# Performance work log

Hardware: AMD Instinct MI355X
Metric: run time of the kernel (lower is better)

Reference implementation:

```python
import jax, jax.numpy as jnp
import numpy as np

B, S, D, H = 8, 1024, 1024, 16
DH = D // H  # 64
SCALE = (DH // H) ** (-0.5)  # faithful to torch: (key.size(-1) // num_heads) ** -0.5 = 4**-0.5 = 0.5
LN_EPS = 1e-5


def setup_inputs() -> dict:
    key = jax.random.key(0)
    ks = jax.random.split(key, 12)
    f = jnp.float32
    return {
        "key":   jax.random.normal(ks[0], (B, S, D), f),
        "value": jax.random.normal(ks[1], (B, S, D), f),
        "query": jax.random.normal(ks[2], (B, S, D), f),
        "Wq": jax.random.normal(ks[3], (D, D), f) * 0.02,
        "bq": jnp.zeros((D,), f),
        "Wk": jax.random.normal(ks[4], (D, D), f) * 0.02,
        "bk": jnp.zeros((D,), f),
        "Wv": jax.random.normal(ks[5], (D, D), f) * 0.02,
        "bv": jnp.zeros((D,), f),
        "Wo": jax.random.normal(ks[6], (D, D), f) * 0.02,
        "bo": jnp.zeros((D,), f),
        "ln_gamma": jnp.ones((D,), f),
        "ln_beta": jnp.zeros((D,), f),
    }


def _layer_norm(x, gamma, beta):
    mu = jnp.mean(x, axis=-1, keepdims=True)
    var = jnp.mean(jnp.square(x - mu), axis=-1, keepdims=True)
    return (x - mu) * jax.lax.rsqrt(var + LN_EPS) * gamma + beta


def reference(key, value, query, Wq, bq, Wk, bk, Wv, bv, Wo, bo, ln_gamma, ln_beta):
    residual = query
    # QKV projections (torch Linear: x @ W.T + b)
    k = key @ Wk.T + bk
    v = value @ Wv.T + bv
    q = query @ Wq.T + bq
    # Faithful raw view [B,S,H*dh] -> [B*H, S, dh] (row-major reshape, as in torch .view)
    k = k.reshape(B * H, S, DH)
    v = v.reshape(B * H, S, DH)
    q = q.reshape(B * H, S, DH)
    # scores: [B*H, S, S], softmax over last axis (dim=2)
    attn = jnp.einsum("bid,bjd->bij", q, k) * SCALE
    attn = jax.nn.softmax(attn, axis=2)
    context = jnp.einsum("bij,bjd->bid", attn, v)
    context = context.reshape(B, S, D)  # faithful raw view back
    out = context @ Wo.T + bo
    out = _layer_norm(residual + out, ln_gamma, ln_beta)
    return out, attn
```

## Files before the change

### kernel.cpp

```cpp
#include <hip/hip_runtime.h>
#include <stdint.h>

typedef unsigned short ushort_t;
typedef __attribute__((ext_vector_type(8))) short s16x8;
typedef __attribute__((ext_vector_type(8))) unsigned short u16x8;
typedef __attribute__((ext_vector_type(4))) unsigned short u16x4;
typedef __attribute__((ext_vector_type(4))) float f32x4;

#define AS1C(p) ((const __attribute__((address_space(1))) void*)(p))
#define AS3(p)  ((__attribute__((address_space(3))) void*)(p))

#define QSCALE 0.7213475204444817f

#define EXP2F(x) __builtin_amdgcn_exp2f(x)
#define LOG2F(x) __builtin_amdgcn_logf(x)

#define WAVE_LDS_FENCE()                                    \
  do {                                                      \
    asm volatile("s_waitcnt lgkmcnt(0)" ::: "memory");      \
    __builtin_amdgcn_sched_barrier(0);                      \
  } while (0)

#define SBAR()                                              \
  do {                                                      \
    __builtin_amdgcn_sched_barrier(0);                      \
    __builtin_amdgcn_s_barrier();                           \
    __builtin_amdgcn_sched_barrier(0);                      \
  } while (0)

__device__ __forceinline__ ushort_t f2bf(float f) {
  uint32_t u = __float_as_uint(f);
  u += 0x7fffu + ((u >> 16) & 1u);
  return (ushort_t)(u >> 16);
}
__device__ __forceinline__ float bf2f(ushort_t h) {
  return __uint_as_float(((uint32_t)h) << 16);
}

__global__ __launch_bounds__(256) void cvt3_kernel(const float* __restrict__ s0,
                                                   const float* __restrict__ s1,
                                                   const float* __restrict__ s2,
                                                   ushort_t* __restrict__ dst) {
  const int y = blockIdx.y;
  const float* src = y == 0 ? s0 : (y == 1 ? s1 : s2);
  const int i = blockIdx.x * 256 + threadIdx.x;
  const float4 v = ((const float4*)src)[i];
  ushort4 o;
  o.x = f2bf(v.x); o.y = f2bf(v.y); o.z = f2bf(v.z); o.w = f2bf(v.w);
  ((ushort4*)(dst + (size_t)y * 8388608))[i] = o;
}

__global__ __launch_bounds__(256) void cvtw_kernel(const float* __restrict__ w0,
                                                   const float* __restrict__ w1,
                                                   const float* __restrict__ w2,
                                                   const float* __restrict__ w3,
                                                   ushort_t* __restrict__ dqkv,
                                                   ushort_t* __restrict__ dwo) {
  const int y = blockIdx.y;
  const float* src = y == 0 ? w0 : (y == 1 ? w1 : (y == 2 ? w2 : w3));
  ushort_t* dst = y < 3 ? dqkv + (size_t)y * 1048576 : dwo;
  const float sc = y == 0 ? QSCALE : 1.0f;
  const int i = blockIdx.x * 256 + threadIdx.x;
  const float4 v = ((const float4*)src)[i];
  ushort4 o;
  o.x = f2bf(v.x * sc); o.y = f2bf(v.y * sc); o.z = f2bf(v.z * sc); o.w = f2bf(v.w * sc);
  ((ushort4*)dst)[i] = o;
}

__global__ __launch_bounds__(256) void biascat_kernel(const float* __restrict__ bq,
                                                      const float* __restrict__ bk,
                                                      const float* __restrict__ bv,
                                                      float* __restrict__ dst) {
  const int i = blockIdx.x * 256 + threadIdx.x;
  dst[i] = i < 1024 ? bq[i] * QSCALE : (i < 2048 ? bk[i - 1024] : bv[i - 2048]);
}

template <int OUT_BF16>
__global__ __launch_bounds__(256) void gemm_nt(const ushort_t* __restrict__ A0,
                                               const ushort_t* __restrict__ A1,
                                               const ushort_t* __restrict__ A2,
                                               const ushort_t* __restrict__ B,
                                               const float* __restrict__ bias,
                                               void* __restrict__ C0,
                                               void* __restrict__ C1,
                                               void* __restrict__ C2) {
  __shared__ ushort_t As[2][128 * 32];
  __shared__ ushort_t Bs[2][128 * 32];
  const int tid = threadIdx.x;
  const int w = tid >> 6, lane = tid & 63, g = lane >> 4, c = lane & 15;
  const int wm = w >> 1, wn = w & 1;
  const int m0 = blockIdx.y * 128, n0 = blockIdx.x * 128;
  const int sel = n0 >> 10, nloc0 = n0 & 1023;
  const ushort_t* A = sel == 0 ? A0 : (sel == 1 ? A1 : A2);
  char* C = (char*)(sel == 0 ? C0 : (sel == 1 ? C1 : C2));
  f32x4 acc[4][4] = {};

  const int row0 = tid >> 2, col0 = (tid & 3) << 3;
  const int row1 = (256 + tid) >> 2, col1 = ((256 + tid) & 3) << 3;
  const int dst0 = (0 * 256 + w * 64) * 8, dst1 = (1 * 256 + w * 64) * 8;

#define G_STAGE(buf, k0_)                                                                  \
  do {                                                                                     \
    __builtin_amdgcn_global_load_lds(AS1C(&A[(size_t)(m0 + row0) * 1024 + (k0_) + col0]),  \
                                     AS3(&As[buf][dst0]), 16, 0, 0);                       \
    __builtin_amdgcn_global_load_lds(AS1C(&B[(size_t)(n0 + row0) * 1024 + (k0_) + col0]),  \
                                     AS3(&Bs[buf][dst0]), 16, 0, 0);                       \
    __builtin_amdgcn_global_load_lds(AS1C(&A[(size_t)(m0 + row1) * 1024 + (k0_) + col1]),  \
                                     AS3(&As[buf][dst1]), 16, 0, 0);                       \
    __builtin_amdgcn_global_load_lds(AS1C(&B[(size_t)(n0 + row1) * 1024 + (k0_) + col1]),  \
                                     AS3(&Bs[buf][dst1]), 16, 0, 0);                       \
  } while (0)

  G_STAGE(0, 0);
  asm volatile("s_waitcnt vmcnt(0)" ::: "memory");
  SBAR();
  for (int it = 0; it < 32; ++it) {
    const int cur = it & 1;
    if (it < 31) G_STAGE(cur ^ 1, 32 * (it + 1));
    s16x8 af[4], bfr[4];
#pragma unroll
    for (int mi = 0; mi < 4; ++mi)
      af[mi] = *(const s16x8*)&As[cur][(wm * 64 + mi * 16 + c) * 32 + g * 8];
#pragma unroll
    for (int ni = 0; ni < 4; ++ni)
      bfr[ni] = *(const s16x8*)&Bs[cur][(wn * 64 + ni * 16 + c) * 32 + g * 8];
    __builtin_amdgcn_s_setprio(1);
#pragma unroll
    for (int mi = 0; mi < 4; ++mi)
#pragma unroll
      for (int ni = 0; ni < 4; ++ni)
        acc[mi][ni] = __builtin_amdgcn_mfma_f32_16x16x32_bf16(af[mi], bfr[ni], acc[mi][ni], 0, 0, 0);
    __builtin_amdgcn_s_setprio(0);
    asm volatile("s_waitcnt vmcnt(0) lgkmcnt(0)" ::: "memory");
    SBAR();
  }
#undef G_STAGE

#pragma unroll
  for (int ni = 0; ni < 4; ++ni) {
    const int nn = wn * 64 + ni * 16 + c;
    const float bv = bias[n0 + nn];
#pragma unroll
    for (int mi = 0; mi < 4; ++mi) {
#pragma unroll
      for (int rr = 0; rr < 4; ++rr) {
        const int m = m0 + wm * 64 + mi * 16 + g * 4 + rr;
        const float val = acc[mi][ni][rr] + bv;
        if (OUT_BF16)
          ((ushort_t*)C)[(size_t)m * 1024 + nloc0 + nn] = f2bf(val);
        else
          ((float*)C)[(size_t)m * 1024 + nloc0 + nn] = val;
      }
    }
  }
}

__global__ __launch_bounds__(256) void transpose_v(const ushort_t* __restrict__ v,
                                                   ushort_t* __restrict__ vt) {
  __shared__ ushort_t T[64][72];
  const int n = blockIdx.y, ib = blockIdx.x;
  const int t = threadIdx.x;
  {
    const int row = t >> 2, cb = (t & 3) << 4;
    const ushort_t* src = v + (size_t)n * 65536 + (size_t)(ib * 64 + row) * 64 + cb;
    *(u16x8*)&T[row][cb] = *(const u16x8*)src;
    *(u16x8*)&T[row][cb + 8] = *(const u16x8*)(src + 8);
  }
  __syncthreads();
  {
    const int dh = t >> 2, ibs = (t & 3) << 4;
    u16x8 a, b;
#pragma unroll
    for (int e = 0; e < 8; ++e) { a[e] = T[ibs + e][dh]; b[e] = T[ibs + 8 + e][dh]; }
    ushort_t* dst = vt + (size_t)n * 65536 + (size_t)dh * 1024 + ib * 64 + ibs;
    *(u16x8*)dst = a;
    *(u16x8*)(dst + 8) = b;
  }
}

__global__ __launch_bounds__(256) void attn_kernel(const ushort_t* __restrict__ q,
                                                   const ushort_t* __restrict__ k,
                                                   const ushort_t* __restrict__ vt,
                                                   float* __restrict__ attn,
                                                   ushort_t* __restrict__ ctx) {
  __shared__ ushort_t Kb[2][64 * 64];
  __shared__ ushort_t Vb[2][64 * 64];
  __shared__ ushort_t Pb[4][16 * 64];
  const int wg = blockIdx.x;
  const int idx = ((wg & 7) << 8) | (wg >> 3);
  const int n = idx >> 4, qb = idx & 15;
  const int tid = threadIdx.x, w = tid >> 6, lane = tid & 63, g = lane >> 4, c = lane & 15;
  const int i0 = qb * 64 + w * 16;
  const ushort_t* qh = q + (size_t)n * 65536;
  const char* khb = (const char*)(k + (size_t)n * 65536);
  const char* vhb = (const char*)(vt + (size_t)n * 65536);
  char* pwb = (char*)&Pb[w][0];

  const int r0 = w * 16 + (lane >> 3);
  const int csw = (((lane & 7) ^ (lane >> 3)) << 4);

#define STAGE_K(buf, jt_)                                                                   \
  do {                                                                                      \
    __builtin_amdgcn_global_load_lds(AS1C(khb + ((size_t)(jt_)*64 + r0) * 128 + csw),       \
                                     AS3(&Kb[buf][(w * 2 + 0) * 512]), 16, 0, 0);           \
    __builtin_amdgcn_global_load_lds(AS1C(khb + ((size_t)(jt_)*64 + r0 + 8) * 128 + csw),   \
                                     AS3(&Kb[buf][(w * 2 + 1) * 512]), 16, 0, 0);           \
  } while (0)
#define STAGE_V(buf, jt_)                                                                   \
  do {                                                                                      \
    __builtin_amdgcn_global_load_lds(AS1C(vhb + (size_t)r0 * 2048 + (jt_)*128 + csw),       \
                                     AS3(&Vb[buf][(w * 2 + 0) * 512]), 16, 0, 0);           \
    __builtin_amdgcn_global_load_lds(AS1C(vhb + (size_t)(r0 + 8) * 2048 + (jt_)*128 + csw), \
                                     AS3(&Vb[buf][(w * 2 + 1) * 512]), 16, 0, 0);           \
  } while (0)
#define KFRAG(buf, jn, h)                                                     \
  (*(const s16x8*)((const char*)&Kb[buf][0] +                                 \
                   (((((jn)*16 + c) * 128 + (h)*64 + g * 16)) ^ ((c & 7) << 4))))
#define VFRAG(buf, dn, ks_)                                                   \
  (*(const s16x8*)((const char*)&Vb[buf][0] +                                 \
                   (((((dn)*16 + c) * 128 + (ks_)*64 + g * 16)) ^ ((c & 7) << 4))))

  const s16x8 aq0 = *(const s16x8*)&qh[(i0 + c) * 64 + g * 8];
  const s16x8 aq1 = *(const s16x8*)&qh[(i0 + c) * 64 + 32 + g * 8];

  float m_p[4], l_p[4];
#pragma unroll
  for (int r = 0; r < 4; ++r) { m_p[r] = -1e30f; l_p[r] = 0.f; }

  STAGE_K(0, 0);
  asm volatile("s_waitcnt vmcnt(0)" ::: "memory");
  SBAR();
  for (int jt = 0; jt < 16; ++jt) {
    const int cur = jt & 1;
    if (jt < 15) STAGE_K(cur ^ 1, jt + 1);
    f32x4 s[4];
    __builtin_amdgcn_s_setprio(1);
#pragma unroll
    for (int jn = 0; jn < 4; ++jn) {
      f32x4 z = {0.f, 0.f, 0.f, 0.f};
      z = __builtin_amdgcn_mfma_f32_16x16x32_bf16(aq0, KFRAG(cur, jn, 0), z, 0, 0, 0);
      z = __builtin_amdgcn_mfma_f32_16x16x32_bf16(aq1, KFRAG(cur, jn, 1), z, 0, 0, 0);
      s[jn] = z;
    }
    __builtin_amdgcn_s_setprio(0);
#pragma unroll
    for (int r = 0; r < 4; ++r) {
      const float pm = fmaxf(fmaxf(s[0][r], s[1][r]), fmaxf(s[2][r], s[3][r]));
      const float mn = fmaxf(m_p[r], pm);
      l_p[r] = l_p[r] * EXP2F(m_p[r] - mn) + EXP2F(s[0][r] - mn) + EXP2F(s[1][r] - mn) +
               EXP2F(s[2][r] - mn) + EXP2F(s[3][r] - mn);
      m_p[r] = mn;
    }
    if (jt < 15) {
      asm volatile("s_waitcnt vmcnt(0) lgkmcnt(0)" ::: "memory");
      SBAR();
    }
  }

  float bias_r[4];
#pragma unroll
  for (int r = 0; r < 4; ++r) {
    float m = m_p[r], l = l_p[r];
#pragma unroll
    for (int mask = 1; mask < 16; mask <<= 1) {
      const float mo = __shfl_xor(m, mask);
      const float lo = __shfl_xor(l, mask);
      const float mn = fmaxf(m, mo);
      l = l * EXP2F(m - mn) + lo * EXP2F(mo - mn);
      m = mn;
    }
    bias_r[r] = m + LOG2F(l);
  }

  f32x4 cacc[4] = {};
  float* arow = attn + (size_t)n * 1048576;

  STAGE_K(0, 0);
  STAGE_V(0, 0);
  asm volatile("s_waitcnt vmcnt(0) lgkmcnt(0)" ::: "memory");
  SBAR();
  for (int jt = 0; jt < 16; ++jt) {
    const int cur = jt & 1;
    if (jt < 15) { STAGE_K(cur ^ 1, jt + 1); STAGE_V(cur ^ 1, jt + 1); }
    f32x4 s[4];
    __builtin_amdgcn_s_setprio(1);
#pragma unroll
    for (int jn = 0; jn < 4; ++jn) {
      f32x4 z = {0.f, 0.f, 0.f, 0.f};
      z = __builtin_amdgcn_mfma_f32_16x16x32_bf16(aq0, KFRAG(cur, jn, 0), z, 0, 0, 0);
      z = __builtin_amdgcn_mfma_f32_16x16x32_bf16(aq1, KFRAG(cur, jn, 1), z, 0, 0, 0);
      s[jn] = z;
    }
    __builtin_amdgcn_s_setprio(0);
#pragma unroll
    for (int jn = 0; jn < 4; ++jn) {
#pragma unroll
      for (int r = 0; r < 4; ++r) {
        const float p = EXP2F(s[jn][r] - bias_r[r]);
        const int row = 4 * g + r;
        const int A = (row << 7) + ((jn * 16 + c) << 1);
        *(ushort_t*)(pwb + (A ^ ((row & 7) << 4))) = f2bf(p);
      }
    }
    WAVE_LDS_FENCE();
    __builtin_amdgcn_s_setprio(1);
#pragma unroll
    for (int ks = 0; ks < 2; ++ks) {
      const int A = (c << 7) + (ks << 6) + (g << 4);
      const s16x8 pa = *(const s16x8*)(pwb + (A ^ ((c & 7) << 4)));
#pragma unroll
      for (int dn = 0; dn < 4; ++dn)
        cacc[dn] = __builtin_amdgcn_mfma_f32_16x16x32_bf16(pa, VFRAG(cur, dn, ks), cacc[dn], 0, 0, 0);
    }
    __builtin_amdgcn_s_setprio(0);
#pragma unroll
    for (int e = 0; e < 4; ++e) {
      const int row = g + 4 * e;
      const int A = (row << 7) + (c << 3);
      const u16x4 hv = *(const u16x4*)(pwb + (A ^ ((row & 7) << 4)));
      f32x4 fv;
#pragma unroll
      for (int t2 = 0; t2 < 4; ++t2) fv[t2] = bf2f(hv[t2]);
      *(f32x4*)&arow[(size_t)(i0 + row) * 1024 + jt * 64 + c * 4] = fv;
    }
    if (jt < 15) {
      asm volatile("s_waitcnt vmcnt(4) lgkmcnt(0)" ::: "memory");
      SBAR();
    }
  }

  ushort_t* ch = ctx + (size_t)n * 65536;
#pragma unroll
  for (int dn = 0; dn < 4; ++dn)
#pragma unroll
    for (int r = 0; r < 4; ++r)
      ch[(size_t)(i0 + 4 * g + r) * 64 + dn * 16 + c] = f2bf(cacc[dn][r]);
#undef STAGE_K
#undef STAGE_V
#undef KFRAG
#undef VFRAG
}

__global__ __launch_bounds__(256) void ln_kernel(const float* __restrict__ proj,
                                                 const float* __restrict__ resid,
                                                 const float* __restrict__ gamma,
                                                 const float* __restrict__ beta,
                                                 float* __restrict__ out) {
  __shared__ float sred[4], ssred[4];
  const int row = blockIdx.x, t = threadIdx.x;
  const float4 pv = ((const float4*)(proj + (size_t)row * 1024))[t];
  const float4 rv = ((const float4*)(resid + (size_t)row * 1024))[t];
  float4 x;
  x.x = pv.x + rv.x; x.y = pv.y + rv.y; x.z = pv.z + rv.z; x.w = pv.w + rv.w;
  float s = x.x + x.y + x.z + x.w;
  float ss = x.x * x.x + x.y * x.y + x.z * x.z + x.w * x.w;
#pragma unroll
  for (int msk = 1; msk < 64; msk <<= 1) {
    s += __shfl_xor(s, msk);
    ss += __shfl_xor(ss, msk);
  }
  const int w = t >> 6, lane = t & 63;
  if (lane == 0) { sred[w] = s; ssred[w] = ss; }
  __syncthreads();
  s = sred[0] + sred[1] + sred[2] + sred[3];
  ss = ssred[0] + ssred[1] + ssred[2] + ssred[3];
  const float mu = s * (1.f / 1024.f);
  const float var = ss * (1.f / 1024.f) - mu * mu;
  const float rs = rsqrtf(var + 1e-5f);
  const float4 gm = ((const float4*)gamma)[t];
  const float4 bt = ((const float4*)beta)[t];
  float4 o;
  o.x = (x.x - mu) * rs * gm.x + bt.x;
  o.y = (x.y - mu) * rs * gm.y + bt.y;
  o.z = (x.z - mu) * rs * gm.z + bt.z;
  o.w = (x.w - mu) * rs * gm.w + bt.w;
  ((float4*)(out + (size_t)row * 1024))[t] = o;
}

extern "C" void kernel_launch(void* const* d_in, const int* in_sizes, int n_in,
                              void* d_out, int out_size, void* d_ws, size_t ws_size,
                              hipStream_t stream) {
  const float* key   = (const float*)d_in[0];
  const float* value = (const float*)d_in[1];
  const float* query = (const float*)d_in[2];
  const float* Wq = (const float*)d_in[3];  const float* bq = (const float*)d_in[4];
  const float* Wk = (const float*)d_in[5];  const float* bk = (const float*)d_in[6];
  const float* Wv = (const float*)d_in[7];  const float* bv = (const float*)d_in[8];
  const float* Wo = (const float*)d_in[9];  const float* bo = (const float*)d_in[10];
  const float* gamma = (const float*)d_in[11];
  const float* beta  = (const float*)d_in[12];

  char* ws = (char*)d_ws;
  ushort_t* q_   = (ushort_t*)(ws + 0);
  ushort_t* k_   = (ushort_t*)(ws + 16777216);
  ushort_t* vt_  = (ushort_t*)(ws + 33554432);
  ushort_t* ctx_ = (ushort_t*)(ws + 50331648);
  ushort_t* wo_  = (ushort_t*)(ws + 67108864);
  float*    proj_ = (float*)(ws + 0);

  char* o8 = (char*)d_out;
  float*    outp  = (float*)o8;
  float*    attnp = (float*)(o8 + 33554432);
  ushort_t* xq   = (ushort_t*)(o8 + 33554432);
  ushort_t* xk   = (ushort_t*)(o8 + 50331648);
  ushort_t* xv   = (ushort_t*)(o8 + 67108864);
  ushort_t* wqkv = (ushort_t*)(o8 + 83886080);
  ushort_t* v_   = (ushort_t*)(o8 + 90177536);
  float*    bqkv = (float*)(o8 + 106954752);

  cvt3_kernel<<<dim3(8192, 3), 256, 0, stream>>>(query, key, value, xq);
  cvtw_kernel<<<dim3(1024, 4), 256, 0, stream>>>(Wq, Wk, Wv, Wo, wqkv, wo_);
  biascat_kernel<<<12, 256, 0, stream>>>(bq, bk, bv, bqkv);

  gemm_nt<1><<<dim3(24, 64), 256, 0, stream>>>(xq, xk, xv, wqkv, bqkv, q_, k_, v_);

  transpose_v<<<dim3(16, 128), 256, 0, stream>>>(v_, vt_);

  attn_kernel<<<2048, 256, 0, stream>>>(q_, k_, vt_, attnp, ctx_);

  gemm_nt<0><<<dim3(8, 64), 256, 0, stream>>>(ctx_, ctx_, ctx_, wo_, bo, proj_, proj_, proj_);

  ln_kernel<<<8192, 256, 0, stream>>>(proj_, query, gamma, beta, outp);
}
```

Measured before the change: 361.3 us.

## Split attention keys across waves with single-pass softmax; triple-buffer GEMM loads

The attention kernel now gives each workgroup 16 query rows and splits the 1024 keys across four waves, 256 keys per wave. Each wave keeps all of its scores in registers, so the score GEMM runs once instead of twice for the two-pass softmax. Row max and sum are combined across waves through LDS, and partial context sums are reduced through LDS before the bf16 store. K and V are now read straight from global memory rather than staged in LDS, and the grid grows to 8192 blocks. Separately, the GEMM moves from double to triple buffering so loads run two stages ahead, at the cost of more LDS and register pressure.

```diff
diff --git a/kernel.cpp b/kernel.cpp
--- a/kernel.cpp
+++ b/kernel.cpp
@@ -84,8 +84,8 @@
                                                void* __restrict__ C0,
                                                void* __restrict__ C1,
                                                void* __restrict__ C2) {
-  __shared__ ushort_t As[2][128 * 32];
-  __shared__ ushort_t Bs[2][128 * 32];
+  __shared__ ushort_t As[3][128 * 32];
+  __shared__ ushort_t Bs[3][128 * 32];
   const int tid = threadIdx.x;
   const int w = tid >> 6, lane = tid & 63, g = lane >> 4, c = lane & 15;
   const int wm = w >> 1, wn = w & 1;
@@ -112,11 +112,15 @@
   } while (0)
 
   G_STAGE(0, 0);
-  asm volatile("s_waitcnt vmcnt(0)" ::: "memory");
+  G_STAGE(1, 32);
+  asm volatile("s_waitcnt vmcnt(4)" ::: "memory");
   SBAR();
+  int cur = 0;
   for (int it = 0; it < 32; ++it) {
-    const int cur = it & 1;
-    if (it < 31) G_STAGE(cur ^ 1, 32 * (it + 1));
+    if (it < 30) {
+      const int sb = cur >= 1 ? cur - 1 : 2;
+      G_STAGE(sb, 32 * (it + 2));
+    }
     s16x8 af[4], bfr[4];
 #pragma unroll
     for (int mi = 0; mi < 4; ++mi)
@@ -131,8 +135,14 @@
       for (int ni = 0; ni < 4; ++ni)
         acc[mi][ni] = __builtin_amdgcn_mfma_f32_16x16x32_bf16(af[mi], bfr[ni], acc[mi][ni], 0, 0, 0);
     __builtin_amdgcn_s_setprio(0);
-    asm volatile("s_waitcnt vmcnt(0) lgkmcnt(0)" ::: "memory");
-    SBAR();
+    if (it < 31) {
+      if (it < 30)
+        asm volatile("s_waitcnt vmcnt(4) lgkmcnt(0)" ::: "memory");
+      else
+        asm volatile("s_waitcnt vmcnt(0) lgkmcnt(0)" ::: "memory");
+      SBAR();
+    }
+    cur = cur < 2 ? cur + 1 : 0;
   }
 #undef G_STAGE
 
@@ -183,162 +193,137 @@
                                                    const ushort_t* __restrict__ vt,
                                                    float* __restrict__ attn,
                                                    ushort_t* __restrict__ ctx) {
-  __shared__ ushort_t Kb[2][64 * 64];
-  __shared__ ushort_t Vb[2][64 * 64];
-  __shared__ ushort_t Pb[4][16 * 64];
+  __shared__ char Lds[4][8192];
+  __shared__ float mlb[4][16][2];
   const int wg = blockIdx.x;
-  const int idx = ((wg & 7) << 8) | (wg >> 3);
-  const int n = idx >> 4, qb = idx & 15;
+  const int idx = ((wg & 7) << 10) | (wg >> 3);
+  const int n = idx >> 6, qb = idx & 63;
   const int tid = threadIdx.x, w = tid >> 6, lane = tid & 63, g = lane >> 4, c = lane & 15;
-  const int i0 = qb * 64 + w * 16;
+  const int i0 = qb * 16;
+  const int cb = w << 8;
   const ushort_t* qh = q + (size_t)n * 65536;
-  const char* khb = (const char*)(k + (size_t)n * 65536);
-  const char* vhb = (const char*)(vt + (size_t)n * 65536);
-  char* pwb = (char*)&Pb[w][0];
-
-  const int r0 = w * 16 + (lane >> 3);
-  const int csw = (((lane & 7) ^ (lane >> 3)) << 4);
-
-#define STAGE_K(buf, jt_)                                                                   \
-  do {                                                                                      \
-    __builtin_amdgcn_global_load_lds(AS1C(khb + ((size_t)(jt_)*64 + r0) * 128 + csw),       \
-                                     AS3(&Kb[buf][(w * 2 + 0) * 512]), 16, 0, 0);           \
-    __builtin_amdgcn_global_load_lds(AS1C(khb + ((size_t)(jt_)*64 + r0 + 8) * 128 + csw),   \
-                                     AS3(&Kb[buf][(w * 2 + 1) * 512]), 16, 0, 0);           \
-  } while (0)
-#define STAGE_V(buf, jt_)                                                                   \
-  do {                                                                                      \
-    __builtin_amdgcn_global_load_lds(AS1C(vhb + (size_t)r0 * 2048 + (jt_)*128 + csw),       \
-                                     AS3(&Vb[buf][(w * 2 + 0) * 512]), 16, 0, 0);           \
-    __builtin_amdgcn_global_load_lds(AS1C(vhb + (size_t)(r0 + 8) * 2048 + (jt_)*128 + csw), \
-                                     AS3(&Vb[buf][(w * 2 + 1) * 512]), 16, 0, 0);           \
-  } while (0)
-#define KFRAG(buf, jn, h)                                                     \
-  (*(const s16x8*)((const char*)&Kb[buf][0] +                                 \
-                   (((((jn)*16 + c) * 128 + (h)*64 + g * 16)) ^ ((c & 7) << 4))))
-#define VFRAG(buf, dn, ks_)                                                   \
-  (*(const s16x8*)((const char*)&Vb[buf][0] +                                 \
-                   (((((dn)*16 + c) * 128 + (ks_)*64 + g * 16)) ^ ((c & 7) << 4))))
+  const ushort_t* kh = k + (size_t)n * 65536;
+  const ushort_t* vh = vt + (size_t)n * 65536;
+  char* pwb = &Lds[w][0];
 
   const s16x8 aq0 = *(const s16x8*)&qh[(i0 + c) * 64 + g * 8];
   const s16x8 aq1 = *(const s16x8*)&qh[(i0 + c) * 64 + 32 + g * 8];
 
-  float m_p[4], l_p[4];
-#pragma unroll
-  for (int r = 0; r < 4; ++r) { m_p[r] = -1e30f; l_p[r] = 0.f; }
-
-  STAGE_K(0, 0);
-  asm volatile("s_waitcnt vmcnt(0)" ::: "memory");
-  SBAR();
-  for (int jt = 0; jt < 16; ++jt) {
-    const int cur = jt & 1;
-    if (jt < 15) STAGE_K(cur ^ 1, jt + 1);
-    f32x4 s[4];
-    __builtin_amdgcn_s_setprio(1);
-#pragma unroll
-    for (int jn = 0; jn < 4; ++jn) {
-      f32x4 z = {0.f, 0.f, 0.f, 0.f};
-      z = __builtin_amdgcn_mfma_f32_16x16x32_bf16(aq0, KFRAG(cur, jn, 0), z, 0, 0, 0);
-      z = __builtin_amdgcn_mfma_f32_16x16x32_bf16(aq1, KFRAG(cur, jn, 1), z, 0, 0, 0);
-      s[jn] = z;
-    }
-    __builtin_amdgcn_s_setprio(0);
+  f32x4 s[16];
+#pragma unroll
+  for (int jn = 0; jn < 16; ++jn) {
+    const ushort_t* kr = &kh[(size_t)(cb + jn * 16 + c) * 64];
+    f32x4 z = {0.f, 0.f, 0.f, 0.f};
+    z = __builtin_amdgcn_mfma_f32_16x16x32_bf16(aq0, *(const s16x8*)&kr[g * 8], z, 0, 0, 0);
+    z = __builtin_amdgcn_mfma_f32_16x16x32_bf16(aq1, *(const s16x8*)&kr[32 + g * 8], z, 0, 0, 0);
+    s[jn] = z;
+  }
+
+  float bias_r[4];
+  {
+    float mr[4], lr[4];
 #pragma unroll
     for (int r = 0; r < 4; ++r) {
-      const float pm = fmaxf(fmaxf(s[0][r], s[1][r]), fmaxf(s[2][r], s[3][r]));
-      const float mn = fmaxf(m_p[r], pm);
-      l_p[r] = l_p[r] * EXP2F(m_p[r] - mn) + EXP2F(s[0][r] - mn) + EXP2F(s[1][r] - mn) +
-               EXP2F(s[2][r] - mn) + EXP2F(s[3][r] - mn);
-      m_p[r] = mn;
-    }
-    if (jt < 15) {
-      asm volatile("s_waitcnt vmcnt(0) lgkmcnt(0)" ::: "memory");
-      SBAR();
-    }
-  }
-
-  float bias_r[4];
-#pragma unroll
-  for (int r = 0; r < 4; ++r) {
-    float m = m_p[r], l = l_p[r];
-#pragma unroll
-    for (int mask = 1; mask < 16; mask <<= 1) {
-      const float mo = __shfl_xor(m, mask);
-      const float lo = __shfl_xor(l, mask);
-      const float mn = fmaxf(m, mo);
-      l = l * EXP2F(m - mn) + lo * EXP2F(mo - mn);
-      m = mn;
-    }
-    bias_r[r] = m + LOG2F(l);
-  }
+      float m = s[0][r];
+#pragma unroll
+      for (int jn = 1; jn < 16; ++jn) m = fmaxf(m, s[jn][r]);
+      m = fmaxf(m, __shfl_xor(m, 1));
+      m = fmaxf(m, __shfl_xor(m, 2));
+      m = fmaxf(m, __shfl_xor(m, 4));
+      m = fmaxf(m, __shfl_xor(m, 8));
+      float l = 0.f;
+#pragma unroll
+      for (int jn = 0; jn < 16; ++jn) l += EXP2F(s[jn][r] - m);
+      l += __shfl_xor(l, 1);
+      l += __shfl_xor(l, 2);
+      l += __shfl_xor(l, 4);
+      l += __shfl_xor(l, 8);
+      mr[r] = m; lr[r] = l;
+    }
+    if (c == 0) {
+#pragma unroll
+      for (int r = 0; r < 4; ++r) {
+        mlb[w][4 * g + r][0] = mr[r];
+        mlb[w][4 * g + r][1] = lr[r];
+      }
+    }
+    WAVE_LDS_FENCE();
+    SBAR();
+#pragma unroll
+    for (int r = 0; r < 4; ++r) {
+      const int row = 4 * g + r;
+      float M = fmaxf(fmaxf(mlb[0][row][0], mlb[1][row][0]),
+                      fmaxf(mlb[2][row][0], mlb[3][row][0]));
+      float L = mlb[0][row][1] * EXP2F(mlb[0][row][0] - M) +
+                mlb[1][row][1] * EXP2F(mlb[1][row][0] - M) +
+                mlb[2][row][1] * EXP2F(mlb[2][row][0] - M) +
+                mlb[3][row][1] * EXP2F(mlb[3][row][0] - M);
+      bias_r[r] = M + LOG2F(L);
+    }
+  }
+
+#pragma unroll
+  for (int jn = 0; jn < 16; ++jn) {
+#pragma unroll
+    for (int r = 0; r < 4; ++r) {
+      const float p = EXP2F(s[jn][r] - bias_r[r]);
+      const int row = 4 * g + r;
+      const int A = (row << 9) + ((jn * 16 + c) << 1);
+      *(ushort_t*)(pwb + (A ^ ((row & 7) << 4))) = f2bf(p);
+    }
+  }
+  WAVE_LDS_FENCE();
 
   f32x4 cacc[4] = {};
+  __builtin_amdgcn_s_setprio(1);
+#pragma unroll
+  for (int kb = 0; kb < 8; ++kb) {
+    const int A = (c << 9) + (kb << 6) + (g << 4);
+    const s16x8 pa = *(const s16x8*)(pwb + (A ^ ((c & 7) << 4)));
+#pragma unroll
+    for (int dn = 0; dn < 4; ++dn) {
+      const s16x8 bv = *(const s16x8*)&vh[(size_t)(dn * 16 + c) * 1024 + cb + kb * 32 + g * 8];
+      cacc[dn] = __builtin_amdgcn_mfma_f32_16x16x32_bf16(pa, bv, cacc[dn], 0, 0, 0);
+    }
+  }
+  __builtin_amdgcn_s_setprio(0);
+
   float* arow = attn + (size_t)n * 1048576;
-
-  STAGE_K(0, 0);
-  STAGE_V(0, 0);
-  asm volatile("s_waitcnt vmcnt(0) lgkmcnt(0)" ::: "memory");
-  SBAR();
-  for (int jt = 0; jt < 16; ++jt) {
-    const int cur = jt & 1;
-    if (jt < 15) { STAGE_K(cur ^ 1, jt + 1); STAGE_V(cur ^ 1, jt + 1); }
-    f32x4 s[4];
-    __builtin_amdgcn_s_setprio(1);
-#pragma unroll
-    for (int jn = 0; jn < 4; ++jn) {
-      f32x4 z = {0.f, 0.f, 0.f, 0.f};
-      z = __builtin_amdgcn_mfma_f32_16x16x32_bf16(aq0, KFRAG(cur, jn, 0), z, 0, 0, 0);
-      z = __builtin_amdgcn_mfma_f32_16x16x32_bf16(aq1, KFRAG(cur, jn, 1), z, 0, 0, 0);
-      s[jn] = z;
-    }
-    __builtin_amdgcn_s_setprio(0);
-#pragma unroll
-    for (int jn = 0; jn < 4; ++jn) {
-#pragma unroll
-      for (int r = 0; r < 4; ++r) {
-        const float p = EXP2F(s[jn][r] - bias_r[r]);
-        const int row = 4 * g + r;
-        const int A = (row << 7) + ((jn * 16 + c) << 1);
-        *(ushort_t*)(pwb + (A ^ ((row & 7) << 4))) = f2bf(p);
-      }
-    }
-    WAVE_LDS_FENCE();
-    __builtin_amdgcn_s_setprio(1);
-#pragma unroll
-    for (int ks = 0; ks < 2; ++ks) {
-      const int A = (c << 7) + (ks << 6) + (g << 4);
-      const s16x8 pa = *(const s16x8*)(pwb + (A ^ ((c & 7) << 4)));
-#pragma unroll
-      for (int dn = 0; dn < 4; ++dn)
-        cacc[dn] = __builtin_amdgcn_mfma_f32_16x16x32_bf16(pa, VFRAG(cur, dn, ks), cacc[dn], 0, 0, 0);
-    }
-    __builtin_amdgcn_s_setprio(0);
+#pragma unroll
+  for (int ch_ = 0; ch_ < 4; ++ch_) {
 #pragma unroll
     for (int e = 0; e < 4; ++e) {
       const int row = g + 4 * e;
-      const int A = (row << 7) + (c << 3);
+      const int A = (row << 9) + (ch_ << 7) + (c << 3);
       const u16x4 hv = *(const u16x4*)(pwb + (A ^ ((row & 7) << 4)));
       f32x4 fv;
 #pragma unroll
       for (int t2 = 0; t2 < 4; ++t2) fv[t2] = bf2f(hv[t2]);
-      *(f32x4*)&arow[(size_t)(i0 + row) * 1024 + jt * 64 + c * 4] = fv;
-    }
-    if (jt < 15) {
-      asm volatile("s_waitcnt vmcnt(4) lgkmcnt(0)" ::: "memory");
-      SBAR();
-    }
-  }
-
-  ushort_t* ch = ctx + (size_t)n * 65536;
+      *(f32x4*)&arow[(size_t)(i0 + row) * 1024 + cb + ch_ * 64 + c * 4] = fv;
+    }
+  }
+  WAVE_LDS_FENCE();
+
+  float* cpart = (float*)pwb;
 #pragma unroll
   for (int dn = 0; dn < 4; ++dn)
 #pragma unroll
     for (int r = 0; r < 4; ++r)
-      ch[(size_t)(i0 + 4 * g + r) * 64 + dn * 16 + c] = f2bf(cacc[dn][r]);
-#undef STAGE_K
-#undef STAGE_V
-#undef KFRAG
-#undef VFRAG
+      cpart[(4 * g + r) * 64 + dn * 16 + c] = cacc[dn][r];
+  WAVE_LDS_FENCE();
+  SBAR();
+  {
+    const int row = tid >> 4, d0 = (tid & 15) << 2;
+    const int off = (row * 64 + d0) * 4;
+    f32x4 t0 = *(const f32x4*)&Lds[0][off];
+    const f32x4 t1 = *(const f32x4*)&Lds[1][off];
+    const f32x4 t2 = *(const f32x4*)&Lds[2][off];
+    const f32x4 t3 = *(const f32x4*)&Lds[3][off];
+    t0 = t0 + t1 + t2 + t3;
+    ushort4 o;
+    o.x = f2bf(t0[0]); o.y = f2bf(t0[1]); o.z = f2bf(t0[2]); o.w = f2bf(t0[3]);
+    *(ushort4*)&ctx[(size_t)n * 65536 + (size_t)(i0 + row) * 64 + d0] = o;
+  }
 }
 
 __global__ __launch_bounds__(256) void ln_kernel(const float* __restrict__ proj,
@@ -416,7 +401,7 @@
 
   transpose_v<<<dim3(16, 128), 256, 0, stream>>>(v_, vt_);
 
-  attn_kernel<<<2048, 256, 0, stream>>>(q_, k_, vt_, attnp, ctx_);
+  attn_kernel<<<8192, 256, 0, stream>>>(q_, k_, vt_, attnp, ctx_);
 
   gemm_nt<0><<<dim3(8, 64), 256, 0, stream>>>(ctx_, ctx_, ctx_, wo_, bo, proj_, proj_, proj_);
 
```

After: 536.4 us. +48.4%, slower.
